# Kernel tuning notes

Measured on AMD Instinct MI355X. Metric: run time of the kernel, lower is better.

## Reference

```python
import jax, jax.numpy as jnp
import numpy as np

B, V = 8, 128  # batch, cubic volume side


def setup_inputs() -> dict:
    key = jax.random.key(0)
    k1, k2 = jax.random.split(key)
    input_volume1 = jax.random.normal(k1, (B, V, V, V), dtype=jnp.float32)
    input_volume2 = jax.random.normal(k2, (B, V, V, V), dtype=jnp.float32)
    return {"input_volume1": input_volume1, "input_volume2": input_volume2}


def reference(input_volume1, input_volume2):
    # Full circular 3D cross-correlation over all relative shifts:
    #   out[b, t] = sum_r v1[b, r] * v2[b, (r + t) mod V]  (t, r are 3D indices)
    # computed via the convolution theorem with real FFTs.
    axes = (1, 2, 3)
    f1 = jnp.fft.rfftn(input_volume1, axes=axes)          # [B, V, V, V//2+1] complex
    f2 = jnp.fft.rfftn(input_volume2, axes=axes)
    out = jnp.fft.irfftn(f1 * jnp.conj(f2), s=(V, V, V), axes=axes)
    return out.astype(jnp.float32)
```

## Files before the change

kernel.cpp:

```cpp
#include <hip/hip_runtime.h>
#include <math.h>


#define V    128
#define V2   16384
#define V3   2097152
#define NB   8
#define PFP  132
#define PH2  68
#define TILE2 (V * PH2)

__device__ __forceinline__ int bitrev7(int x) {
  return (int)(__brev((unsigned)x) >> 25);
}
__device__ __forceinline__ int negrev(int j) {
  int k = bitrev7(j);
  return bitrev7((V - k) & (V - 1));
}

__device__ __forceinline__ float2 cmul(float2 a, float2 b) {
  return make_float2(a.x * b.x - a.y * b.y, a.x * b.y + a.y * b.x);
}
__device__ __forceinline__ float2 cmulc(float2 a, float2 b) {
  return make_float2(a.x * b.x + a.y * b.y, a.y * b.x - a.x * b.y);
}
__device__ __forceinline__ float2 csqr(float2 a) {
  return make_float2(a.x * a.x - a.y * a.y, 2.0f * a.x * a.y);
}
__device__ __forceinline__ float2 f2add(float2 a, float2 b) {
  return make_float2(a.x + b.x, a.y + b.y);
}
__device__ __forceinline__ float2 f2sub(float2 a, float2 b) {
  return make_float2(a.x - b.x, a.y - b.y);
}
__device__ __forceinline__ float2 NI(float2 z) { return make_float2(z.y, -z.x); }
__device__ __forceinline__ float2 PI(float2 z) { return make_float2(-z.y, z.x); }

template <int CTRL>
__device__ __forceinline__ float dppf(float v) {
  return __int_as_float(
      __builtin_amdgcn_update_dpp(0, __float_as_int(v), CTRL, 0xF, 0xF, true));
}
template <int CTRL>
__device__ __forceinline__ float2 dpp2(float2 v) {
  return make_float2(dppf<CTRL>(v.x), dppf<CTRL>(v.y));
}

struct WF16 {
  float2 T64[4], T32[2], T16a, T16b, T8w, ts4, ts2;
  float sg4, sg2, sg1;
  bool up4, up2;
  int e;

  __device__ void init(int lq) {
    e = lq ^ (((lq >> 2) & 1) * 3);
    const float k = -6.28318530717958647692f / 128.0f;
    float2 w1 = make_float2(cosf(k * (float)e), sinf(k * (float)e));
    const float C1 = 0.92387953251128675613f;
    const float S1 = 0.38268343236508977173f;
    const float R  = 0.70710678118654752440f;
    T64[0] = w1;
    T64[1] = cmul(w1, make_float2(C1, -S1));
    T64[2] = cmul(w1, make_float2(R, -R));
    T64[3] = cmul(w1, make_float2(S1, -C1));
    float2 w2 = csqr(w1);
    T32[0] = w2;
    T32[1] = cmul(w2, make_float2(R, -R));
    T16a = csqr(w2);
    T16b = NI(T16a);
    T8w = csqr(T16a);
    up4 = (e >> 2) & 1;
    up2 = (e >> 1) & 1;
    const bool up1 = e & 1;
    sg4 = up4 ? -1.0f : 1.0f;
    sg2 = up2 ? -1.0f : 1.0f;
    sg1 = up1 ? -1.0f : 1.0f;
    const int m4 = e & 3;
    float2 w8p = (m4 == 0) ? make_float2(1.0f, 0.0f)
               : (m4 == 1) ? make_float2(R, -R)
               : (m4 == 2) ? make_float2(0.0f, -1.0f)
                           : make_float2(-R, -R);
    ts4 = up4 ? w8p : make_float2(1.0f, 0.0f);
    ts2 = (up2 && (e & 1)) ? make_float2(0.0f, -1.0f) : make_float2(1.0f, 0.0f);
  }

  __device__ __forceinline__ void fwd(float2 c[16]) const {
#pragma unroll
    for (int j = 0; j < 8; ++j) {
      float2 u = c[j], v = c[j + 8];
      c[j] = f2add(u, v);
      float2 t = cmul(f2sub(u, v), T64[j & 3]);
      c[j + 8] = (j < 4) ? t : NI(t);
    }
#pragma unroll
    for (int g = 0; g < 2; ++g) {
#pragma unroll
      for (int j0 = 0; j0 < 4; ++j0) {
        const int j = g * 8 + j0;
        float2 u = c[j], v = c[j + 4];
        c[j] = f2add(u, v);
        float2 t = cmul(f2sub(u, v), T32[j0 & 1]);
        c[j + 4] = (j0 < 2) ? t : NI(t);
      }
    }
#pragma unroll
    for (int g = 0; g < 4; ++g) {
#pragma unroll
      for (int j0 = 0; j0 < 2; ++j0) {
        const int j = g * 4 + j0;
        float2 u = c[j], v = c[j + 2];
        c[j] = f2add(u, v);
        c[j + 2] = cmul(f2sub(u, v), j0 ? T16b : T16a);
      }
    }
#pragma unroll
    for (int j = 0; j < 16; j += 2) {
      float2 u = c[j], v = c[j + 1];
      c[j] = f2add(u, v);
      c[j + 1] = cmul(f2sub(u, v), T8w);
    }
#pragma unroll
    for (int j = 0; j < 16; ++j) {
      float2 p = dpp2<0x141>(c[j]);
      float2 t = make_float2(fmaf(c[j].x, sg4, p.x), fmaf(c[j].y, sg4, p.y));
      c[j] = cmul(t, ts4);
    }
#pragma unroll
    for (int j = 0; j < 16; ++j) {
      float2 p = dpp2<0x4E>(c[j]);
      float2 t = make_float2(fmaf(c[j].x, sg2, p.x), fmaf(c[j].y, sg2, p.y));
      c[j] = cmul(t, ts2);
    }
#pragma unroll
    for (int j = 0; j < 16; ++j) {
      float2 p = dpp2<0xB1>(c[j]);
      c[j] = make_float2(fmaf(c[j].x, sg1, p.x), fmaf(c[j].y, sg1, p.y));
    }
  }

  __device__ __forceinline__ void inv(float2 c[16]) const {
#pragma unroll
    for (int j = 0; j < 16; ++j) {
      float2 p = dpp2<0xB1>(c[j]);
      c[j] = make_float2(fmaf(c[j].x, sg1, p.x), fmaf(c[j].y, sg1, p.y));
    }
#pragma unroll
    for (int j = 0; j < 16; ++j) {
      float2 m = cmulc(c[j], ts2);
      float2 q = make_float2(up2 ? m.x : c[j].x, up2 ? m.y : c[j].y);
      float2 p = dpp2<0x4E>(q);
      c[j] = make_float2(fmaf(q.x, sg2, p.x), fmaf(q.y, sg2, p.y));
    }
#pragma unroll
    for (int j = 0; j < 16; ++j) {
      float2 m = cmulc(c[j], ts4);
      float2 q = make_float2(up4 ? m.x : c[j].x, up4 ? m.y : c[j].y);
      float2 p = dpp2<0x141>(q);
      c[j] = make_float2(fmaf(q.x, sg4, p.x), fmaf(q.y, sg4, p.y));
    }
#pragma unroll
    for (int j = 0; j < 16; j += 2) {
      float2 m = cmulc(c[j + 1], T8w);
      float2 u = c[j];
      c[j] = f2add(u, m);
      c[j + 1] = f2sub(u, m);
    }
#pragma unroll
    for (int g = 0; g < 4; ++g) {
#pragma unroll
      for (int j0 = 0; j0 < 2; ++j0) {
        const int j = g * 4 + j0;
        float2 m = cmulc(c[j + 2], j0 ? T16b : T16a);
        float2 u = c[j];
        c[j] = f2add(u, m);
        c[j + 2] = f2sub(u, m);
      }
    }
#pragma unroll
    for (int g = 0; g < 2; ++g) {
#pragma unroll
      for (int j0 = 0; j0 < 4; ++j0) {
        const int j = g * 8 + j0;
        float2 m0 = cmulc(c[j + 4], T32[j0 & 1]);
        float2 m = (j0 < 2) ? m0 : PI(m0);
        float2 u = c[j];
        c[j] = f2add(u, m);
        c[j + 4] = f2sub(u, m);
      }
    }
#pragma unroll
    for (int j = 0; j < 8; ++j) {
      float2 m0 = cmulc(c[j + 8], T64[j & 3]);
      float2 m = (j < 4) ? m0 : PI(m0);
      float2 u = c[j];
      c[j] = f2add(u, m);
      c[j + 8] = f2sub(u, m);
    }
  }
};

__global__ __launch_bounds__(1024) void k_fwd_xy(const float* __restrict__ v1,
                                                 const float* __restrict__ v2,
                                                 float2* __restrict__ Z) {
  __shared__ float2 s[V * PFP];
  const int tid = threadIdx.x, lane = tid & 63, wave = tid >> 6;
  const int o = lane >> 3, lq = lane & 7;
  const int b = blockIdx.x >> 7, z1 = blockIdx.x & 127;
  WF16 F;
  F.init(lq);
  const int e = F.e;
  float2 c[16];
  {
    const int y = wave * 8 + o;
    const size_t g = (size_t)b * V3 + (size_t)z1 * V2 + (size_t)y * V;
#pragma unroll
    for (int j = 0; j < 16; ++j) {
      const int n = e + 8 * j;
      c[j] = make_float2(v1[g + n], v2[g + n]);
    }
    F.fwd(c);
#pragma unroll
    for (int j = 0; j < 16; ++j) s[y * PFP + e + 8 * j] = c[j];
  }
  __syncthreads();
  {
    const int x = wave * 8 + o;
#pragma unroll
    for (int j = 0; j < 16; ++j) c[j] = s[(e + 8 * j) * PFP + x];
    F.fwd(c);
    const size_t zb = ((size_t)(b * V + x) * V + z1) * V;
#pragma unroll
    for (int j = 0; j < 16; ++j) Z[zb + e + 8 * j] = c[j];
  }
}

__global__ __launch_bounds__(1024) void k_z_fused(float2* __restrict__ Z) {
  __shared__ float2 T[2 * TILE2];
  const int tid = threadIdx.x, lane = tid & 63, wave = tid >> 6;
  const int o = lane >> 3, lq = lane & 7;
  const int blk = blockIdx.x;
  const int b = blk / 130, r = blk % 130, g = r >> 1, yh = r & 1;
  int xA, xB;
  if (g < 2) {
    xA = xB = g;
  } else {
    const int k = g - 1;
    xA = bitrev7(k);
    xB = bitrev7(V - k);
  }
  const bool self = (xA == xB);
  WF16 F;
  F.init(lq);
  const int e = F.e;
  const size_t baseA = (size_t)(b * V + xA) * V2 + yh * 64;
  const size_t baseB = (size_t)(b * V + xB) * V2 + yh * 64;

  for (int p = tid; p < 4096; p += 1024) {
    const int z = p >> 5, y = (p & 31) << 1;
    *(float4*)&T[z * PH2 + y] = *(const float4*)&Z[baseA + (size_t)z * V + y];
  }
  if (!self) {
    for (int p = tid; p < 4096; p += 1024) {
      const int z = p >> 5, y = (p & 31) << 1;
      *(float4*)&T[TILE2 + z * PH2 + y] =
          *(const float4*)&Z[baseB + (size_t)z * V + y];
    }
  }
  __syncthreads();

  const int col = wave * 8 + o;
  const int tb = (col >> 6) * TILE2;
  const int yc = col & 63;
  const bool active = (!self) || (wave < 8);
  float2 c[16];
  if (active) {
#pragma unroll
    for (int j = 0; j < 16; ++j) c[j] = T[tb + (e + 8 * j) * PH2 + yc];
    F.fwd(c);
#pragma unroll
    for (int j = 0; j < 16; ++j) T[tb + (e + 8 * j) * PH2 + yc] = c[j];
  }
  __syncthreads();

  if (!self) {
    for (int p = tid; p < 8192; p += 1024) {
      const int z = p >> 6, y = p & 63;
      const int zm = negrev(z), ym = negrev(yh * 64 + y) & 63;
      const float2 a  = T[z * PH2 + y];
      const float2 bb = T[TILE2 + zm * PH2 + ym];
      const float f1r = 0.5f * (a.x + bb.x), f1i = 0.5f * (a.y - bb.y);
      const float f2r = 0.5f * (a.y + bb.y), f2i = 0.5f * (bb.x - a.x);
      const float gr = f1r * f2r + f1i * f2i;
      const float gi = f1i * f2r - f1r * f2i;
      T[z * PH2 + y] = make_float2(gr, gi);
      T[TILE2 + zm * PH2 + ym] = make_float2(gr, -gi);
    }
  } else {
    for (int p = tid; p < 8192; p += 1024) {
      const int z = p >> 6, y = p & 63;
      const int zm = negrev(z), ym = negrev(yh * 64 + y) & 63;
      const int pm = zm * 64 + ym;
      if (pm < p) continue;
      const float2 a  = T[z * PH2 + y];
      const float2 bb = T[zm * PH2 + ym];
      const float f1r = 0.5f * (a.x + bb.x), f1i = 0.5f * (a.y - bb.y);
      const float f2r = 0.5f * (a.y + bb.y), f2i = 0.5f * (bb.x - a.x);
      const float gr = f1r * f2r + f1i * f2i;
      const float gi = f1i * f2r - f1r * f2i;
      T[z * PH2 + y] = make_float2(gr, gi);
      if (pm != p) T[zm * PH2 + ym] = make_float2(gr, -gi);
    }
  }
  __syncthreads();

  if (active) {
#pragma unroll
    for (int j = 0; j < 16; ++j) c[j] = T[tb + (e + 8 * j) * PH2 + yc];
    F.inv(c);
#pragma unroll
    for (int j = 0; j < 16; ++j) T[tb + (e + 8 * j) * PH2 + yc] = c[j];
  }
  __syncthreads();

  for (int p = tid; p < 4096; p += 1024) {
    const int z = p >> 5, y = (p & 31) << 1;
    *(float4*)&Z[baseA + (size_t)z * V + y] = *(const float4*)&T[z * PH2 + y];
  }
  if (!self) {
    for (int p = tid; p < 4096; p += 1024) {
      const int z = p >> 5, y = (p & 31) << 1;
      *(float4*)&Z[baseB + (size_t)z * V + y] =
          *(const float4*)&T[TILE2 + z * PH2 + y];
    }
  }
}

__global__ __launch_bounds__(1024) void k_inv_xy(const float2* __restrict__ Z,
                                                 float* __restrict__ out) {
  __shared__ float2 s[V * PFP];
  const int tid = threadIdx.x, lane = tid & 63, wave = tid >> 6;
  const int o = lane >> 3, lq = lane & 7;
  const int b = blockIdx.x >> 7, z1 = blockIdx.x & 127;
  WF16 F;
  F.init(lq);
  const int e = F.e;
  float2 c[16];
  {
    const int x = wave * 8 + o;
    const size_t zb = ((size_t)(b * V + x) * V + z1) * V;
#pragma unroll
    for (int j = 0; j < 16; ++j) c[j] = Z[zb + e + 8 * j];
    F.inv(c);
#pragma unroll
    for (int j = 0; j < 16; ++j) s[(e + 8 * j) * PFP + x] = c[j];
  }
  __syncthreads();
  const float sc = 1.0f / 2097152.0f;
  {
    const int y = wave * 8 + o;
#pragma unroll
    for (int j = 0; j < 16; ++j) c[j] = s[y * PFP + e + 8 * j];
    F.inv(c);
    const size_t gg = (size_t)b * V3 + (size_t)z1 * V2 + (size_t)y * V;
#pragma unroll
    for (int j = 0; j < 16; ++j) out[gg + e + 8 * j] = c[j].x * sc;
  }
}

extern "C" void kernel_launch(void* const* d_in, const int* in_sizes, int n_in,
                              void* d_out, int out_size, void* d_ws, size_t ws_size,
                              hipStream_t stream) {
  const float* v1 = (const float*)d_in[0];
  const float* v2 = (const float*)d_in[1];
  float* out = (float*)d_out;
  float2* Z  = (float2*)d_ws;

  k_fwd_xy<<<NB * V, 1024, 0, stream>>>(v1, v2, Z);
  k_z_fused<<<NB * 130, 1024, 0, stream>>>(Z);
  k_inv_xy<<<NB * V, 1024, 0, stream>>>(Z, out);
}
```

Measured before the change: 316.5 us.

## Process two z-planes per block with prefetch and split z-pass into smaller blocks

The xy forward and inverse kernels now handle two consecutive z-planes per block. Global loads for the second plane are issued before the first plane's second FFT pass, so memory latency overlaps with compute. The z-pass kernel is reorganized into 512-thread blocks over 32-column slices with a new pairing of conjugate-symmetric x columns, which balances work and raises occupancy. The cost is more register pressure in the xy kernels and half as many blocks there, which may reduce parallelism.

```diff
diff --git a/kernel.cpp b/kernel.cpp
--- a/kernel.cpp
+++ b/kernel.cpp
@@ -7,8 +7,8 @@
 #define V3   2097152
 #define NB   8
 #define PFP  132
-#define PH2  68
-#define TILE2 (V * PH2)
+#define PH3  34
+#define SLICE (V * PH3)
 
 __device__ __forceinline__ int bitrev7(int x) {
   return (int)(__brev((unsigned)x) >> 25);
@@ -205,14 +205,15 @@
   __shared__ float2 s[V * PFP];
   const int tid = threadIdx.x, lane = tid & 63, wave = tid >> 6;
   const int o = lane >> 3, lq = lane & 7;
-  const int b = blockIdx.x >> 7, z1 = blockIdx.x & 127;
+  const int b = blockIdx.x >> 6, zp = blockIdx.x & 63;
+  const int z1 = zp * 2;
   WF16 F;
   F.init(lq);
   const int e = F.e;
+  const int row = wave * 8 + o;
   float2 c[16];
   {
-    const int y = wave * 8 + o;
-    const size_t g = (size_t)b * V3 + (size_t)z1 * V2 + (size_t)y * V;
+    const size_t g = (size_t)b * V3 + (size_t)z1 * V2 + (size_t)row * V;
 #pragma unroll
     for (int j = 0; j < 16; ++j) {
       const int n = e + 8 * j;
@@ -220,118 +221,142 @@
     }
     F.fwd(c);
 #pragma unroll
-    for (int j = 0; j < 16; ++j) s[y * PFP + e + 8 * j] = c[j];
-  }
-  __syncthreads();
-  {
-    const int x = wave * 8 + o;
-#pragma unroll
-    for (int j = 0; j < 16; ++j) c[j] = s[(e + 8 * j) * PFP + x];
+    for (int j = 0; j < 16; ++j) s[row * PFP + e + 8 * j] = c[j];
+  }
+  __syncthreads();
+  float pa[16], pb[16];
+  {
+    const size_t g = (size_t)b * V3 + (size_t)(z1 + 1) * V2 + (size_t)row * V;
+#pragma unroll
+    for (int j = 0; j < 16; ++j) {
+      const int n = e + 8 * j;
+      pa[j] = v1[g + n];
+      pb[j] = v2[g + n];
+    }
+  }
+  {
+    float2 d[16];
+#pragma unroll
+    for (int j = 0; j < 16; ++j) d[j] = s[(e + 8 * j) * PFP + row];
+    F.fwd(d);
+    const size_t zb = ((size_t)(b * V + row) * V + z1) * V;
+#pragma unroll
+    for (int j = 0; j < 16; ++j) Z[zb + e + 8 * j] = d[j];
+  }
+  __syncthreads();
+  {
+#pragma unroll
+    for (int j = 0; j < 16; ++j) c[j] = make_float2(pa[j], pb[j]);
     F.fwd(c);
-    const size_t zb = ((size_t)(b * V + x) * V + z1) * V;
-#pragma unroll
-    for (int j = 0; j < 16; ++j) Z[zb + e + 8 * j] = c[j];
-  }
-}
-
-__global__ __launch_bounds__(1024) void k_z_fused(float2* __restrict__ Z) {
-  __shared__ float2 T[2 * TILE2];
+#pragma unroll
+    for (int j = 0; j < 16; ++j) s[row * PFP + e + 8 * j] = c[j];
+  }
+  __syncthreads();
+  {
+    float2 d[16];
+#pragma unroll
+    for (int j = 0; j < 16; ++j) d[j] = s[(e + 8 * j) * PFP + row];
+    F.fwd(d);
+    const size_t zb = ((size_t)(b * V + row) * V + (z1 + 1)) * V;
+#pragma unroll
+    for (int j = 0; j < 16; ++j) Z[zb + e + 8 * j] = d[j];
+  }
+}
+
+__global__ __launch_bounds__(512, 4) void k_z_fused(float2* __restrict__ Z) {
+  __shared__ float2 T[2 * SLICE];
   const int tid = threadIdx.x, lane = tid & 63, wave = tid >> 6;
   const int o = lane >> 3, lq = lane & 7;
   const int blk = blockIdx.x;
-  const int b = blk / 130, r = blk % 130, g = r >> 1, yh = r & 1;
-  int xA, xB;
-  if (g < 2) {
-    xA = xB = g;
-  } else {
-    const int k = g - 1;
-    xA = bitrev7(k);
-    xB = bitrev7(V - k);
-  }
-  const bool self = (xA == xB);
+  const int b = blk >> 8, idx = blk & 255;
+  int x0, x1, jb0, jb1;
+  bool within = false;
+  {
+    const int h = idx >> 7, r2 = idx & 127;
+    if (r2 < 126) {
+      const int k = (r2 >> 1) + 1, cc = r2 & 1;
+      const int xa = bitrev7(k), xb = bitrev7(V - k);
+      if (h == 0) { x0 = xa; x1 = xb; jb0 = cc * 32; jb1 = cc * 32; }
+      else { x0 = cc ? xb : xa; x1 = cc ? xa : xb; jb0 = 64; jb1 = 96; }
+    } else {
+      x0 = x1 = r2 - 126;
+      if (h == 0) { jb0 = 0; jb1 = 32; within = true; }
+      else { jb0 = 64; jb1 = 96; }
+    }
+  }
   WF16 F;
   F.init(lq);
   const int e = F.e;
-  const size_t baseA = (size_t)(b * V + xA) * V2 + yh * 64;
-  const size_t baseB = (size_t)(b * V + xB) * V2 + yh * 64;
-
-  for (int p = tid; p < 4096; p += 1024) {
-    const int z = p >> 5, y = (p & 31) << 1;
-    *(float4*)&T[z * PH2 + y] = *(const float4*)&Z[baseA + (size_t)z * V + y];
-  }
-  if (!self) {
-    for (int p = tid; p < 4096; p += 1024) {
-      const int z = p >> 5, y = (p & 31) << 1;
-      *(float4*)&T[TILE2 + z * PH2 + y] =
-          *(const float4*)&Z[baseB + (size_t)z * V + y];
-    }
+  const size_t base0 = (size_t)(b * V + x0) * V2 + jb0;
+  const size_t base1 = (size_t)(b * V + x1) * V2 + jb1;
+
+  for (int p = tid; p < 2048; p += 512) {
+    const int z = p >> 4, w = (p & 15) << 1;
+    *(float4*)&T[z * PH3 + w] = *(const float4*)&Z[base0 + (size_t)z * V + w];
+  }
+  for (int p = tid; p < 2048; p += 512) {
+    const int z = p >> 4, w = (p & 15) << 1;
+    *(float4*)&T[SLICE + z * PH3 + w] =
+        *(const float4*)&Z[base1 + (size_t)z * V + w];
   }
   __syncthreads();
 
   const int col = wave * 8 + o;
-  const int tb = (col >> 6) * TILE2;
-  const int yc = col & 63;
-  const bool active = (!self) || (wave < 8);
+  const int tb = (col >> 5) * SLICE, yc = col & 31;
   float2 c[16];
-  if (active) {
-#pragma unroll
-    for (int j = 0; j < 16; ++j) c[j] = T[tb + (e + 8 * j) * PH2 + yc];
-    F.fwd(c);
-#pragma unroll
-    for (int j = 0; j < 16; ++j) T[tb + (e + 8 * j) * PH2 + yc] = c[j];
-  }
-  __syncthreads();
-
-  if (!self) {
-    for (int p = tid; p < 8192; p += 1024) {
-      const int z = p >> 6, y = p & 63;
-      const int zm = negrev(z), ym = negrev(yh * 64 + y) & 63;
-      const float2 a  = T[z * PH2 + y];
-      const float2 bb = T[TILE2 + zm * PH2 + ym];
+#pragma unroll
+  for (int j = 0; j < 16; ++j) c[j] = T[tb + (e + 8 * j) * PH3 + yc];
+  F.fwd(c);
+#pragma unroll
+  for (int j = 0; j < 16; ++j) T[tb + (e + 8 * j) * PH3 + yc] = c[j];
+  __syncthreads();
+
+  if (!within) {
+    for (int p = tid; p < 4096; p += 512) {
+      const int z = p >> 5, t = p & 31;
+      const int zm = negrev(z), tm = negrev(jb0 + t) & 31;
+      const float2 a  = T[z * PH3 + t];
+      const float2 bb = T[SLICE + zm * PH3 + tm];
       const float f1r = 0.5f * (a.x + bb.x), f1i = 0.5f * (a.y - bb.y);
       const float f2r = 0.5f * (a.y + bb.y), f2i = 0.5f * (bb.x - a.x);
       const float gr = f1r * f2r + f1i * f2i;
       const float gi = f1i * f2r - f1r * f2i;
-      T[z * PH2 + y] = make_float2(gr, gi);
-      T[TILE2 + zm * PH2 + ym] = make_float2(gr, -gi);
+      T[z * PH3 + t] = make_float2(gr, gi);
+      T[SLICE + zm * PH3 + tm] = make_float2(gr, -gi);
     }
   } else {
-    for (int p = tid; p < 8192; p += 1024) {
-      const int z = p >> 6, y = p & 63;
-      const int zm = negrev(z), ym = negrev(yh * 64 + y) & 63;
-      const int pm = zm * 64 + ym;
-      if (pm < p) continue;
-      const float2 a  = T[z * PH2 + y];
-      const float2 bb = T[zm * PH2 + ym];
+    for (int p = tid; p < 8192; p += 512) {
+      const int s2 = p >> 12, z = (p >> 5) & 127, t = p & 31;
+      const int zm = negrev(z), tm = negrev(s2 * 32 + t) & 31;
+      const int pl = z * 32 + t, pm = zm * 32 + tm;
+      if (pm < pl) continue;
+      const float2 a  = T[s2 * SLICE + z * PH3 + t];
+      const float2 bb = T[s2 * SLICE + zm * PH3 + tm];
       const float f1r = 0.5f * (a.x + bb.x), f1i = 0.5f * (a.y - bb.y);
       const float f2r = 0.5f * (a.y + bb.y), f2i = 0.5f * (bb.x - a.x);
       const float gr = f1r * f2r + f1i * f2i;
       const float gi = f1i * f2r - f1r * f2i;
-      T[z * PH2 + y] = make_float2(gr, gi);
-      if (pm != p) T[zm * PH2 + ym] = make_float2(gr, -gi);
-    }
-  }
-  __syncthreads();
-
-  if (active) {
-#pragma unroll
-    for (int j = 0; j < 16; ++j) c[j] = T[tb + (e + 8 * j) * PH2 + yc];
-    F.inv(c);
-#pragma unroll
-    for (int j = 0; j < 16; ++j) T[tb + (e + 8 * j) * PH2 + yc] = c[j];
-  }
-  __syncthreads();
-
-  for (int p = tid; p < 4096; p += 1024) {
-    const int z = p >> 5, y = (p & 31) << 1;
-    *(float4*)&Z[baseA + (size_t)z * V + y] = *(const float4*)&T[z * PH2 + y];
-  }
-  if (!self) {
-    for (int p = tid; p < 4096; p += 1024) {
-      const int z = p >> 5, y = (p & 31) << 1;
-      *(float4*)&Z[baseB + (size_t)z * V + y] =
-          *(const float4*)&T[TILE2 + z * PH2 + y];
-    }
+      T[s2 * SLICE + z * PH3 + t] = make_float2(gr, gi);
+      if (pm != pl) T[s2 * SLICE + zm * PH3 + tm] = make_float2(gr, -gi);
+    }
+  }
+  __syncthreads();
+
+#pragma unroll
+  for (int j = 0; j < 16; ++j) c[j] = T[tb + (e + 8 * j) * PH3 + yc];
+  F.inv(c);
+#pragma unroll
+  for (int j = 0; j < 16; ++j) T[tb + (e + 8 * j) * PH3 + yc] = c[j];
+  __syncthreads();
+
+  for (int p = tid; p < 2048; p += 512) {
+    const int z = p >> 4, w = (p & 15) << 1;
+    *(float4*)&Z[base0 + (size_t)z * V + w] = *(const float4*)&T[z * PH3 + w];
+  }
+  for (int p = tid; p < 2048; p += 512) {
+    const int z = p >> 4, w = (p & 15) << 1;
+    *(float4*)&Z[base1 + (size_t)z * V + w] =
+        *(const float4*)&T[SLICE + z * PH3 + w];
   }
 }
 
@@ -340,30 +365,53 @@
   __shared__ float2 s[V * PFP];
   const int tid = threadIdx.x, lane = tid & 63, wave = tid >> 6;
   const int o = lane >> 3, lq = lane & 7;
-  const int b = blockIdx.x >> 7, z1 = blockIdx.x & 127;
+  const int b = blockIdx.x >> 6, zp = blockIdx.x & 63;
+  const int z1 = zp * 2;
   WF16 F;
   F.init(lq);
   const int e = F.e;
+  const int row = wave * 8 + o;
+  const float sc = 1.0f / 2097152.0f;
   float2 c[16];
-  {
-    const int x = wave * 8 + o;
-    const size_t zb = ((size_t)(b * V + x) * V + z1) * V;
-#pragma unroll
-    for (int j = 0; j < 16; ++j) c[j] = Z[zb + e + 8 * j];
+  const size_t zb0 = ((size_t)(b * V + row) * V + z1) * V;
+  {
+#pragma unroll
+    for (int j = 0; j < 16; ++j) c[j] = Z[zb0 + e + 8 * j];
     F.inv(c);
 #pragma unroll
-    for (int j = 0; j < 16; ++j) s[(e + 8 * j) * PFP + x] = c[j];
-  }
-  __syncthreads();
-  const float sc = 1.0f / 2097152.0f;
-  {
-    const int y = wave * 8 + o;
-#pragma unroll
-    for (int j = 0; j < 16; ++j) c[j] = s[y * PFP + e + 8 * j];
-    F.inv(c);
-    const size_t gg = (size_t)b * V3 + (size_t)z1 * V2 + (size_t)y * V;
-#pragma unroll
-    for (int j = 0; j < 16; ++j) out[gg + e + 8 * j] = c[j].x * sc;
+    for (int j = 0; j < 16; ++j) s[(e + 8 * j) * PFP + row] = c[j];
+  }
+  __syncthreads();
+  float2 pz[16];
+  {
+    const size_t zb1 = zb0 + V;
+#pragma unroll
+    for (int j = 0; j < 16; ++j) pz[j] = Z[zb1 + e + 8 * j];
+  }
+  {
+    float2 d[16];
+#pragma unroll
+    for (int j = 0; j < 16; ++j) d[j] = s[row * PFP + e + 8 * j];
+    F.inv(d);
+    const size_t gg = (size_t)b * V3 + (size_t)z1 * V2 + (size_t)row * V;
+#pragma unroll
+    for (int j = 0; j < 16; ++j) out[gg + e + 8 * j] = d[j].x * sc;
+  }
+  __syncthreads();
+  {
+    F.inv(pz);
+#pragma unroll
+    for (int j = 0; j < 16; ++j) s[(e + 8 * j) * PFP + row] = pz[j];
+  }
+  __syncthreads();
+  {
+    float2 d[16];
+#pragma unroll
+    for (int j = 0; j < 16; ++j) d[j] = s[row * PFP + e + 8 * j];
+    F.inv(d);
+    const size_t gg = (size_t)b * V3 + (size_t)(z1 + 1) * V2 + (size_t)row * V;
+#pragma unroll
+    for (int j = 0; j < 16; ++j) out[gg + e + 8 * j] = d[j].x * sc;
   }
 }
 
@@ -375,7 +423,7 @@
   float* out = (float*)d_out;
   float2* Z  = (float2*)d_ws;
 
-  k_fwd_xy<<<NB * V, 1024, 0, stream>>>(v1, v2, Z);
-  k_z_fused<<<NB * 130, 1024, 0, stream>>>(Z);
-  k_inv_xy<<<NB * V, 1024, 0, stream>>>(Z, out);
-}
+  k_fwd_xy<<<NB * 64, 1024, 0, stream>>>(v1, v2, Z);
+  k_z_fused<<<NB * 256, 512, 0, stream>>>(Z);
+  k_inv_xy<<<NB * 64, 1024, 0, stream>>>(Z, out);
+}
```

Result: no change. 310.8 us (-1.8%).
